# Optimization experiments

Measured on AMD Instinct MI355X. Metric: run time of the kernel, lower is better.

## Reference

```python
import jax, jax.numpy as jnp
import numpy as np


def setup_inputs() -> dict:
    key = jax.random.key(0)
    ks = jax.random.split(key, 8)
    B, S, D, H, E = 4, 2048, 1024, 2048, 8
    s = 0.02  # init scale
    return {
        "x": jax.random.normal(ks[0], (B, S, D), dtype=jnp.float32),
        "gate_w": jax.random.normal(ks[1], (E, D), dtype=jnp.float32) * s,
        "w1": jax.random.normal(ks[2], (E, H, D), dtype=jnp.float32) * s,
        "b1": jnp.zeros((E, H), dtype=jnp.float32),
        "w2": jax.random.normal(ks[3], (E, H, D), dtype=jnp.float32) * s,
        "b2": jnp.zeros((E, H), dtype=jnp.float32),
        "w3": jax.random.normal(ks[4], (E, D, H), dtype=jnp.float32) * s,
        "b3": jnp.zeros((E, D), dtype=jnp.float32),
        "topk": 2,
    }


def reference(x, gate_w, w1, b1, w2, b2, w3, b3, topk):
    D = x.shape[-1]
    E = gate_w.shape[0]
    xf = x.reshape(-1, D)                      # [T, D]
    T = xf.shape[0]

    logits = xf @ gate_w.T                     # [T, E]
    vals, idx = jax.lax.top_k(logits, topk)    # [T, K]
    wts = jax.nn.softmax(vals, axis=-1)        # [T, K]

    # per-token combine weight per expert (0 if expert not in top-k)
    comb = jnp.zeros((T, E), dtype=xf.dtype).at[
        jnp.arange(T)[:, None], idx
    ].add(wts)                                 # [T, E]

    out = jnp.zeros_like(xf)
    for e in range(E):  # fixed small loop over experts
        h = (xf @ w1[e].T + b1[e]) * jax.nn.silu(xf @ w2[e].T + b2[e])  # [T, H]
        y = h @ w3[e].T + b3[e]                                           # [T, D]
        out = out + comb[:, e:e + 1] * y
    return out.reshape(x.shape)
```

## Files before the change

kernel.cpp:

```cpp
#include <hip/hip_runtime.h>
#include <hip/hip_bf16.h>
#include <stdint.h>

#define T_TOK   8192
#define D_DIM   1024
#define H_DIM   2048
#define E_EXP   8
#define NP2     4096
#define BM      256
#define CAP     (2*T_TOK + E_EXP*BM)
#define MAXMB   (CAP/BM)

using f32x4 = __attribute__((ext_vector_type(4))) float;
using s16x4 = __attribute__((ext_vector_type(4))) short;
using s16x8 = __attribute__((ext_vector_type(8))) short;

__device__ __forceinline__ short bf16_of(float f) {
  union { float f; unsigned u; } v; v.f = f;
  unsigned r = v.u + 0x7FFFu + ((v.u >> 16) & 1u);
  return (short)(r >> 16);
}
__device__ __forceinline__ float f_of_bf16(short s) {
  union { unsigned u; float f; } v; v.u = ((unsigned)(unsigned short)s) << 16;
  return v.f;
}

__device__ __forceinline__ void gload16(const void* g, void* l) {
  __builtin_amdgcn_global_load_lds(
      (const __attribute__((address_space(1))) unsigned int*)g,
      (__attribute__((address_space(3))) unsigned int*)l, 16, 0, 0);
}

__global__ __launch_bounds__(256) void conv_w12(const float* __restrict__ w1,
                                                const float* __restrict__ w2,
                                                short* __restrict__ w12b) {
  int idx = blockIdx.x * 256 + threadIdx.x;
  int e = idx >> 20;
  int rem = idx & 0xFFFFF;
  int np = rem >> 8;
  int kc = rem & 255;
  int g = np >> 5, tt = np & 31, half = tt >> 4, srow = g * 16 + (tt & 15);
  const f32x4* src = (const f32x4*)(half ? w2 : w1) + ((size_t)e * H_DIM + srow) * 256 + kc;
  f32x4 v = *src;
  s16x4 o;
  o[0] = bf16_of(v[0]); o[1] = bf16_of(v[1]); o[2] = bf16_of(v[2]); o[3] = bf16_of(v[3]);
  ((s16x4*)w12b)[idx] = o;
}

__global__ __launch_bounds__(256) void conv_w3(const float* __restrict__ w3,
                                               short* __restrict__ w3b) {
  int idx = blockIdx.x * 256 + threadIdx.x;
  f32x4 v = ((const f32x4*)w3)[idx];
  s16x4 o;
  o[0] = bf16_of(v[0]); o[1] = bf16_of(v[1]); o[2] = bf16_of(v[2]); o[3] = bf16_of(v[3]);
  ((s16x4*)w3b)[idx] = o;
}

__global__ __launch_bounds__(256) void gate_kernel(const float* __restrict__ x,
                                                   const float* __restrict__ gw,
                                                   int* __restrict__ tok_e,
                                                   float* __restrict__ gatew) {
  __shared__ float g[E_EXP * D_DIM];
  int tid = threadIdx.x;
  for (int i = tid; i < E_EXP * 256; i += 256)
    ((f32x4*)g)[i] = ((const f32x4*)gw)[i];
  __syncthreads();
  int w = tid >> 6, lane = tid & 63;
  int t = blockIdx.x * 4 + w;
  float acc[E_EXP] = {};
  const f32x4* xrow = (const f32x4*)(x + (size_t)t * D_DIM);
#pragma unroll
  for (int i = 0; i < 4; ++i) {
    f32x4 xv = xrow[lane + 64 * i];
#pragma unroll
    for (int e = 0; e < E_EXP; ++e) {
      f32x4 gv = ((const f32x4*)g)[e * 256 + lane + 64 * i];
      acc[e] += xv[0] * gv[0] + xv[1] * gv[1] + xv[2] * gv[2] + xv[3] * gv[3];
    }
  }
#pragma unroll
  for (int e = 0; e < E_EXP; ++e)
#pragma unroll
    for (int off = 1; off < 64; off <<= 1)
      acc[e] += __shfl_xor(acc[e], off);
  if (lane == 0) {
    int i0 = 0; float v0 = acc[0];
    for (int e = 1; e < E_EXP; ++e) if (acc[e] > v0) { v0 = acc[e]; i0 = e; }
    int i1 = -1; float v1 = -1e30f;
    for (int e = 0; e < E_EXP; ++e) if (e != i0 && acc[e] > v1) { v1 = acc[e]; i1 = e; }
    float z = __expf(v1 - v0);
    tok_e[2 * t] = i0; tok_e[2 * t + 1] = i1;
    gatew[2 * t] = 1.f / (1.f + z); gatew[2 * t + 1] = z / (1.f + z);
  }
}

__global__ __launch_bounds__(256) void hist_kernel(const int* __restrict__ tok_e,
                                                   int* __restrict__ counts) {
  __shared__ int bc[E_EXP];
  const int tid = threadIdx.x, lane = tid & 63;
  if (tid < E_EXP) bc[tid] = 0;
  __syncthreads();
  const int4 v = ((const int4*)tok_e)[blockIdx.x * 256 + tid];
#pragma unroll
  for (int e = 0; e < E_EXP; ++e) {
    int cnt = __popcll(__ballot(v.x == e)) + __popcll(__ballot(v.y == e)) +
              __popcll(__ballot(v.z == e)) + __popcll(__ballot(v.w == e));
    if (lane == 0 && cnt) atomicAdd(&bc[e], cnt);
  }
  __syncthreads();
  if (tid < E_EXP && bc[tid]) atomicAdd(&counts[tid], bc[tid]);
}

__global__ void scan_kernel(const int* __restrict__ counts, int* __restrict__ off,
                            int* __restrict__ mb2e, int* __restrict__ mb2row) {
  if (threadIdx.x == 0 && blockIdx.x == 0) {
    int acc = 0, mb = 0;
    for (int e = 0; e < E_EXP; ++e) {
      off[e] = acc;
      int nb = (counts[e] + BM - 1) / BM;
      for (int b = 0; b < nb; ++b) { mb2e[mb] = e; mb2row[mb] = acc + b * BM; ++mb; }
      acc += nb * BM;
    }
    off[E_EXP] = acc;
    for (; mb < MAXMB; ++mb) mb2e[mb] = -1;
  }
}

__global__ __launch_bounds__(256) void assign_kernel(const int* __restrict__ tok_e,
                                                     const int* __restrict__ off,
                                                     int* __restrict__ fill,
                                                     int* __restrict__ perm,
                                                     int* __restrict__ tok_slot) {
  __shared__ int wcnt[4][E_EXP];
  __shared__ int wbase[4][E_EXP];
  const int tid = threadIdx.x, lane = tid & 63, wid = tid >> 6;
  if (tid < 32) wcnt[tid >> 3][tid & 7] = 0;
  __syncthreads();
  const int ent = blockIdx.x * 256 + tid;
  const int e = tok_e[ent];
  int myrank = 0;
#pragma unroll
  for (int e0 = 0; e0 < E_EXP; ++e0) {
    unsigned long long m = __ballot(e == e0);
    if (e == e0) {
      myrank = __popcll(m & ((1ull << lane) - 1ull));
      if (myrank == 0) wcnt[wid][e0] = __popcll(m);
    }
  }
  __syncthreads();
  if (tid < E_EXP) {
    int tot = wcnt[0][tid] + wcnt[1][tid] + wcnt[2][tid] + wcnt[3][tid];
    int base = tot ? atomicAdd(&fill[tid], tot) : 0;
#pragma unroll
    for (int w = 0; w < 4; ++w) { wbase[w][tid] = base; base += wcnt[w][tid]; }
  }
  __syncthreads();
  const int slot = off[e] + wbase[wid][e] + myrank;
  perm[slot] = ent >> 1;
  tok_slot[ent] = slot;
}

__global__ __launch_bounds__(128) void gather_kernel(const float* __restrict__ x,
                                                     const int* __restrict__ off,
                                                     const int* __restrict__ counts,
                                                     const int* __restrict__ perm,
                                                     short* __restrict__ Xp) {
  int s = blockIdx.x, tid = threadIdx.x;
  int e = -1;
#pragma unroll
  for (int i = 0; i < E_EXP; ++i)
    if (s >= off[i] && s < off[i + 1]) { e = i; break; }
  bool valid = false; int t = 0;
  if (e >= 0) { int r = s - off[e]; if (r < counts[e]) { valid = true; t = perm[s]; } }
  s16x8 o;
  if (valid) {
    const f32x4* xr = (const f32x4*)(x + (size_t)t * D_DIM);
    f32x4 a = xr[tid * 2], b = xr[tid * 2 + 1];
    o[0] = bf16_of(a[0]); o[1] = bf16_of(a[1]); o[2] = bf16_of(a[2]); o[3] = bf16_of(a[3]);
    o[4] = bf16_of(b[0]); o[5] = bf16_of(b[1]); o[6] = bf16_of(b[2]); o[7] = bf16_of(b[3]);
  } else {
#pragma unroll
    for (int j = 0; j < 8; ++j) o[j] = 0;
  }
  *(s16x8*)(Xp + (size_t)s * D_DIM + tid * 8) = o;
}

template <int K, int BN_, int EPI>
__global__ __launch_bounds__(512, (BN_ == 128) ? 4 : 2)
void gemm256(const short* __restrict__ A,
             const short* __restrict__ Bw,
             const int* __restrict__ mb2e,
             const int* __restrict__ mb2row,
             const float* __restrict__ biasA,
             const float* __restrict__ biasB,
             short* __restrict__ Out) {
  constexpr int NFULL = (EPI == 0) ? NP2 : D_DIM;
  constexpr int OUTLD = (EPI == 0) ? H_DIM : D_DIM;
  constexpr int KB = K * 2;
  constexpr int NT = K / 32;
  constexpr int NBF = BN_ / 64;
  constexpr int ABYTES = 16384;
  constexpr int BBYTES = BN_ * 64;
  constexpr int BUFB = ABYTES + BBYTES;
  constexpr int NB_LOADS = BN_ / 128;
  constexpr int INFLIGHT = 2 + NB_LOADS;

  const int mb = blockIdx.y;
  const int e = mb2e[mb];
  if (e < 0) return;
  const int row0 = mb2row[mb];
  const int bn = blockIdx.x;

  __shared__ alignas(16) char lds[3 * BUFB];

  const int tid = threadIdx.x;
  const int lane = tid & 63;
  const int wid = tid >> 6;
  const int wr = wid >> 2;
  const int wc = wid & 3;

  const char* gA = (const char*)(A + (size_t)row0 * K);
  const char* gB = (const char*)(Bw + ((size_t)e * NFULL + (size_t)bn * BN_) * K);

  const int srow0 = tid >> 2, spq = tid & 3;

  f32x4 acc[8][NBF] = {};

  auto stageA = [&](int kt, int buf) {
#pragma unroll
    for (int r = 0; r < 2; ++r) {
      const int row = r * 128 + srow0;
      const int lq = spq ^ ((row >> 1) & 3);
      gload16(gA + (size_t)row * KB + kt * 64 + lq * 16,
              lds + buf * BUFB + r * 8192 + tid * 16);
    }
  };
  auto stageB = [&](int kt, int buf) {
#pragma unroll
    for (int r = 0; r < NB_LOADS; ++r) {
      const int row = r * 128 + srow0;
      const int lq = spq ^ ((row >> 1) & 3);
      gload16(gB + (size_t)row * KB + kt * 64 + lq * 16,
              lds + buf * BUFB + ABYTES + r * 8192 + tid * 16);
    }
  };

  stageA(0, 0); stageB(0, 0);
  stageA(1, 1); stageB(1, 1);
  if constexpr (BN_ == 256) asm volatile("s_waitcnt vmcnt(4)" ::: "memory");
  else                      asm volatile("s_waitcnt vmcnt(3)" ::: "memory");
  __builtin_amdgcn_s_barrier();
  __builtin_amdgcn_sched_barrier(0);

  const int qsw = (((lane >> 4) ^ ((lane >> 1) & 3)) << 4);
  const int arow = wr * 128 + (lane & 15);
  const int brow = wc * (BN_ / 4) + (lane & 15);

  int bc = 0;
  int b2 = 2;
  for (int t = 0; t < NT; ++t) {
    const char* bufb = lds + bc * BUFB;
    const char* pa = bufb + arow * 64 + qsw;
    const char* pb = bufb + ABYTES + brow * 64 + qsw;
    s16x8 av[4], bv[NBF];
#pragma unroll
    for (int f = 0; f < NBF; ++f) bv[f] = *(const s16x8*)(pb + f * 1024);
#pragma unroll
    for (int f = 0; f < 4; ++f) av[f] = *(const s16x8*)(pa + f * 1024);
    if (t + 2 < NT) stageA(t + 2, b2);
    __builtin_amdgcn_s_setprio(1);
#pragma unroll
    for (int mf = 0; mf < 4; ++mf)
#pragma unroll
      for (int nf = 0; nf < NBF; ++nf)
        acc[mf][nf] = __builtin_amdgcn_mfma_f32_16x16x32_bf16(av[mf], bv[nf], acc[mf][nf], 0, 0, 0);
    __builtin_amdgcn_s_setprio(0);
#pragma unroll
    for (int f = 0; f < 4; ++f) av[f] = *(const s16x8*)(pa + (4 + f) * 1024);
    if (t + 2 < NT) stageB(t + 2, b2);
    __builtin_amdgcn_s_setprio(1);
#pragma unroll
    for (int mf = 0; mf < 4; ++mf)
#pragma unroll
      for (int nf = 0; nf < NBF; ++nf)
        acc[4 + mf][nf] = __builtin_amdgcn_mfma_f32_16x16x32_bf16(av[mf], bv[nf], acc[4 + mf][nf], 0, 0, 0);
    __builtin_amdgcn_s_setprio(0);

    if (t < NT - 1) {
      __builtin_amdgcn_sched_barrier(0);
      if (t == NT - 2)          asm volatile("s_waitcnt vmcnt(0)" ::: "memory");
      else if (BN_ == 256)      asm volatile("s_waitcnt vmcnt(4)" ::: "memory");
      else                      asm volatile("s_waitcnt vmcnt(3)" ::: "memory");
      __builtin_amdgcn_s_barrier();
      __builtin_amdgcn_sched_barrier(0);
    }
    bc = (bc == 2) ? 0 : bc + 1;
    b2 = (b2 == 2) ? 0 : b2 + 1;
  }

  if constexpr (EPI == 0) {
#pragma unroll
    for (int mf = 0; mf < 8; ++mf) {
      const int mrow = row0 + wr * 128 + mf * 16 + ((lane >> 4) << 2);
#pragma unroll
      for (int p = 0; p < 2; ++p) {
        const int hcol = bn * 128 + wc * 32 + p * 16 + (lane & 15);
        const float bb1 = biasA[e * H_DIM + hcol];
        const float bb2 = biasB[e * H_DIM + hcol];
        const f32x4 a1 = acc[mf][2 * p], a2 = acc[mf][2 * p + 1];
#pragma unroll
        for (int j = 0; j < 4; ++j) {
          float x1 = a1[j] + bb1, x2 = a2[j] + bb2;
          float hv = x1 * (x2 / (1.f + __expf(-x2)));
          Out[(size_t)(mrow + j) * OUTLD + hcol] = bf16_of(hv);
        }
      }
    }
  } else {
#pragma unroll
    for (int mf = 0; mf < 8; ++mf) {
      const int mrow = row0 + wr * 128 + mf * 16 + ((lane >> 4) << 2);
#pragma unroll
      for (int nf = 0; nf < NBF; ++nf) {
        const int col = bn * BN_ + wc * (BN_ / 4) + nf * 16 + (lane & 15);
        const float bb = biasA[e * D_DIM + col];
#pragma unroll
        for (int j = 0; j < 4; ++j)
          Out[(size_t)(mrow + j) * OUTLD + col] = bf16_of(acc[mf][nf][j] + bb);
      }
    }
  }
}

__global__ __launch_bounds__(128) void combine_kernel(const short* __restrict__ ysb,
                                                      const int* __restrict__ tok_slot,
                                                      const float* __restrict__ gatew,
                                                      float* __restrict__ out) {
  int t = blockIdx.x, tid = threadIdx.x;
  int s0 = tok_slot[2 * t], s1 = tok_slot[2 * t + 1];
  float w0 = gatew[2 * t], w1 = gatew[2 * t + 1];
  s16x8 a = *(const s16x8*)(ysb + (size_t)s0 * D_DIM + tid * 8);
  s16x8 b = *(const s16x8*)(ysb + (size_t)s1 * D_DIM + tid * 8);
  float* op = out + (size_t)t * D_DIM + tid * 8;
  f32x4 o0, o1;
#pragma unroll
  for (int j = 0; j < 4; ++j) o0[j] = w0 * f_of_bf16(a[j]) + w1 * f_of_bf16(b[j]);
#pragma unroll
  for (int j = 0; j < 4; ++j) o1[j] = w0 * f_of_bf16(a[4 + j]) + w1 * f_of_bf16(b[4 + j]);
  *(f32x4*)op = o0;
  *(f32x4*)(op + 4) = o1;
}

extern "C" void kernel_launch(void* const* d_in, const int* in_sizes, int n_in,
                              void* d_out, int out_size, void* d_ws, size_t ws_size,
                              hipStream_t stream) {
  const float* x  = (const float*)d_in[0];
  const float* gw = (const float*)d_in[1];
  const float* w1 = (const float*)d_in[2];
  const float* b1 = (const float*)d_in[3];
  const float* w2 = (const float*)d_in[4];
  const float* b2 = (const float*)d_in[5];
  const float* w3 = (const float*)d_in[6];
  const float* b3 = (const float*)d_in[7];
  float* out = (float*)d_out;

  char* ws = (char*)d_ws;
  size_t o = 0;
  short* w12b = (short*)(ws + o); o += (size_t)E_EXP * NP2 * D_DIM * 2;
  short* w3b  = (short*)(ws + o); o += (size_t)E_EXP * D_DIM * H_DIM * 2;
  short* Xp   = (short*)(ws + o); o += (size_t)CAP * D_DIM * 2;
  short* ysb  = Xp;
  short* hbuf = (short*)(ws + o); o += (size_t)CAP * H_DIM * 2;
  int* meta     = (int*)(ws + o);
  int* counts   = meta;
  int* fill     = meta + 8;
  int* offv     = meta + 16;
  int* mb2e     = meta + 32;
  int* mb2row   = meta + 112;
  int* tok_e    = meta + 192;
  int* tok_slot = tok_e + 2 * T_TOK;
  int* perm     = tok_slot + 2 * T_TOK;
  float* gatew  = (float*)(perm + CAP);
  const size_t ws_needed = o + (192 + 4 * T_TOK + CAP + 2 * T_TOK) * sizeof(int);
  if (ws_size < ws_needed) return;

  hipMemsetAsync(counts, 0, 16 * sizeof(int), stream);

  conv_w12<<<(E_EXP * NP2 * 256) / 256, 256, 0, stream>>>(w1, w2, w12b);
  conv_w3 <<<(E_EXP * D_DIM * (H_DIM / 4)) / 256, 256, 0, stream>>>(w3, w3b);
  gate_kernel<<<T_TOK / 4, 256, 0, stream>>>(x, gw, tok_e, gatew);
  hist_kernel<<<(2 * T_TOK) / 1024, 256, 0, stream>>>(tok_e, counts);
  scan_kernel<<<1, 64, 0, stream>>>(counts, offv, mb2e, mb2row);
  assign_kernel<<<(2 * T_TOK) / 256, 256, 0, stream>>>(tok_e, offv, fill, perm, tok_slot);
  gather_kernel<<<CAP, 128, 0, stream>>>(x, offv, counts, perm, Xp);
  gemm256<D_DIM, 256, 0><<<dim3(NP2 / 256, MAXMB), 512, 0, stream>>>(Xp, w12b, mb2e, mb2row, b1, b2, hbuf);
  gemm256<H_DIM, 128, 1><<<dim3(D_DIM / 128, MAXMB), 512, 0, stream>>>(hbuf, w3b, mb2e, mb2row, b3, b3, ysb);
  combine_kernel<<<T_TOK, 128, 0, stream>>>(ysb, tok_slot, gatew, out);
}
```

Baseline: 383.5 us.

## Fuse weighted combine into down-projection GEMM epilogue via atomic adds

Removes the separate combine kernel. The second GEMM's epilogue now scales each row by its gate weight and atomically adds it straight into the zero-initialised fp32 output, using the permutation and per-slot weights written by the assign kernel. The down-projection tile width also grows from 128 to 256 columns, with lower occupancy in exchange for more reuse. This drops the bf16 intermediate round trip and one kernel launch, but adds a full output memset, uncoalesced per-element fp32 atomics, and a grid cut to 4 column blocks per row block.

```diff
diff --git a/kernel.cpp b/kernel.cpp
--- a/kernel.cpp
+++ b/kernel.cpp
@@ -127,10 +127,11 @@
 }
 
 __global__ __launch_bounds__(256) void assign_kernel(const int* __restrict__ tok_e,
+                                                     const float* __restrict__ gatew,
                                                      const int* __restrict__ off,
                                                      int* __restrict__ fill,
                                                      int* __restrict__ perm,
-                                                     int* __restrict__ tok_slot) {
+                                                     float* __restrict__ wslot) {
   __shared__ int wcnt[4][E_EXP];
   __shared__ int wbase[4][E_EXP];
   const int tid = threadIdx.x, lane = tid & 63, wid = tid >> 6;
@@ -157,7 +158,7 @@
   __syncthreads();
   const int slot = off[e] + wbase[wid][e] + myrank;
   perm[slot] = ent >> 1;
-  tok_slot[ent] = slot;
+  wslot[slot] = gatew[ent];
 }
 
 __global__ __launch_bounds__(128) void gather_kernel(const float* __restrict__ x,
@@ -185,25 +186,25 @@
   *(s16x8*)(Xp + (size_t)s * D_DIM + tid * 8) = o;
 }
 
-template <int K, int BN_, int EPI>
-__global__ __launch_bounds__(512, (BN_ == 128) ? 4 : 2)
+template <int K, int EPI>
+__global__ __launch_bounds__(512, 2)
 void gemm256(const short* __restrict__ A,
              const short* __restrict__ Bw,
              const int* __restrict__ mb2e,
              const int* __restrict__ mb2row,
              const float* __restrict__ biasA,
              const float* __restrict__ biasB,
-             short* __restrict__ Out) {
+             short* __restrict__ Out,
+             const int* __restrict__ permv,
+             const float* __restrict__ wslot,
+             const int* __restrict__ offv,
+             const int* __restrict__ cnts,
+             float* __restrict__ outp) {
   constexpr int NFULL = (EPI == 0) ? NP2 : D_DIM;
-  constexpr int OUTLD = (EPI == 0) ? H_DIM : D_DIM;
   constexpr int KB = K * 2;
   constexpr int NT = K / 32;
-  constexpr int NBF = BN_ / 64;
   constexpr int ABYTES = 16384;
-  constexpr int BBYTES = BN_ * 64;
-  constexpr int BUFB = ABYTES + BBYTES;
-  constexpr int NB_LOADS = BN_ / 128;
-  constexpr int INFLIGHT = 2 + NB_LOADS;
+  constexpr int BUFB = 2 * ABYTES;
 
   const int mb = blockIdx.y;
   const int e = mb2e[mb];
@@ -220,11 +221,11 @@
   const int wc = wid & 3;
 
   const char* gA = (const char*)(A + (size_t)row0 * K);
-  const char* gB = (const char*)(Bw + ((size_t)e * NFULL + (size_t)bn * BN_) * K);
+  const char* gB = (const char*)(Bw + ((size_t)e * NFULL + (size_t)bn * 256) * K);
 
   const int srow0 = tid >> 2, spq = tid & 3;
 
-  f32x4 acc[8][NBF] = {};
+  f32x4 acc[8][4] = {};
 
   auto stageA = [&](int kt, int buf) {
 #pragma unroll
@@ -237,7 +238,7 @@
   };
   auto stageB = [&](int kt, int buf) {
 #pragma unroll
-    for (int r = 0; r < NB_LOADS; ++r) {
+    for (int r = 0; r < 2; ++r) {
       const int row = r * 128 + srow0;
       const int lq = spq ^ ((row >> 1) & 3);
       gload16(gB + (size_t)row * KB + kt * 64 + lq * 16,
@@ -247,14 +248,13 @@
 
   stageA(0, 0); stageB(0, 0);
   stageA(1, 1); stageB(1, 1);
-  if constexpr (BN_ == 256) asm volatile("s_waitcnt vmcnt(4)" ::: "memory");
-  else                      asm volatile("s_waitcnt vmcnt(3)" ::: "memory");
+  asm volatile("s_waitcnt vmcnt(4)" ::: "memory");
   __builtin_amdgcn_s_barrier();
   __builtin_amdgcn_sched_barrier(0);
 
   const int qsw = (((lane >> 4) ^ ((lane >> 1) & 3)) << 4);
   const int arow = wr * 128 + (lane & 15);
-  const int brow = wc * (BN_ / 4) + (lane & 15);
+  const int brow = wc * 64 + (lane & 15);
 
   int bc = 0;
   int b2 = 2;
@@ -262,9 +262,9 @@
     const char* bufb = lds + bc * BUFB;
     const char* pa = bufb + arow * 64 + qsw;
     const char* pb = bufb + ABYTES + brow * 64 + qsw;
-    s16x8 av[4], bv[NBF];
-#pragma unroll
-    for (int f = 0; f < NBF; ++f) bv[f] = *(const s16x8*)(pb + f * 1024);
+    s16x8 av[4], bv[4];
+#pragma unroll
+    for (int f = 0; f < 4; ++f) bv[f] = *(const s16x8*)(pb + f * 1024);
 #pragma unroll
     for (int f = 0; f < 4; ++f) av[f] = *(const s16x8*)(pa + f * 1024);
     if (t + 2 < NT) stageA(t + 2, b2);
@@ -272,7 +272,7 @@
 #pragma unroll
     for (int mf = 0; mf < 4; ++mf)
 #pragma unroll
-      for (int nf = 0; nf < NBF; ++nf)
+      for (int nf = 0; nf < 4; ++nf)
         acc[mf][nf] = __builtin_amdgcn_mfma_f32_16x16x32_bf16(av[mf], bv[nf], acc[mf][nf], 0, 0, 0);
     __builtin_amdgcn_s_setprio(0);
 #pragma unroll
@@ -282,15 +282,14 @@
 #pragma unroll
     for (int mf = 0; mf < 4; ++mf)
 #pragma unroll
-      for (int nf = 0; nf < NBF; ++nf)
+      for (int nf = 0; nf < 4; ++nf)
         acc[4 + mf][nf] = __builtin_amdgcn_mfma_f32_16x16x32_bf16(av[mf], bv[nf], acc[4 + mf][nf], 0, 0, 0);
     __builtin_amdgcn_s_setprio(0);
 
     if (t < NT - 1) {
       __builtin_amdgcn_sched_barrier(0);
-      if (t == NT - 2)          asm volatile("s_waitcnt vmcnt(0)" ::: "memory");
-      else if (BN_ == 256)      asm volatile("s_waitcnt vmcnt(4)" ::: "memory");
-      else                      asm volatile("s_waitcnt vmcnt(3)" ::: "memory");
+      if (t == NT - 2) asm volatile("s_waitcnt vmcnt(0)" ::: "memory");
+      else             asm volatile("s_waitcnt vmcnt(4)" ::: "memory");
       __builtin_amdgcn_s_barrier();
       __builtin_amdgcn_sched_barrier(0);
     }
@@ -312,43 +311,35 @@
         for (int j = 0; j < 4; ++j) {
           float x1 = a1[j] + bb1, x2 = a2[j] + bb2;
           float hv = x1 * (x2 / (1.f + __expf(-x2)));
-          Out[(size_t)(mrow + j) * OUTLD + hcol] = bf16_of(hv);
+          Out[(size_t)(mrow + j) * H_DIM + hcol] = bf16_of(hv);
         }
       }
     }
   } else {
+    const int ebase = offv[e];
+    const int ecnt = cnts[e];
 #pragma unroll
     for (int mf = 0; mf < 8; ++mf) {
       const int mrow = row0 + wr * 128 + mf * 16 + ((lane >> 4) << 2);
-#pragma unroll
-      for (int nf = 0; nf < NBF; ++nf) {
-        const int col = bn * BN_ + wc * (BN_ / 4) + nf * 16 + (lane & 15);
+      int tok[4]; float wg[4]; bool val[4];
+#pragma unroll
+      for (int j = 0; j < 4; ++j) {
+        const int s = mrow + j;
+        val[j] = (s - ebase) < ecnt;
+        tok[j] = val[j] ? permv[s] : 0;
+        wg[j]  = val[j] ? wslot[s] : 0.f;
+      }
+#pragma unroll
+      for (int nf = 0; nf < 4; ++nf) {
+        const int col = bn * 256 + wc * 64 + nf * 16 + (lane & 15);
         const float bb = biasA[e * D_DIM + col];
 #pragma unroll
         for (int j = 0; j < 4; ++j)
-          Out[(size_t)(mrow + j) * OUTLD + col] = bf16_of(acc[mf][nf][j] + bb);
+          if (val[j])
+            atomicAdd(&outp[(size_t)tok[j] * D_DIM + col], wg[j] * (acc[mf][nf][j] + bb));
       }
     }
   }
-}
-
-__global__ __launch_bounds__(128) void combine_kernel(const short* __restrict__ ysb,
-                                                      const int* __restrict__ tok_slot,
-                                                      const float* __restrict__ gatew,
-                                                      float* __restrict__ out) {
-  int t = blockIdx.x, tid = threadIdx.x;
-  int s0 = tok_slot[2 * t], s1 = tok_slot[2 * t + 1];
-  float w0 = gatew[2 * t], w1 = gatew[2 * t + 1];
-  s16x8 a = *(const s16x8*)(ysb + (size_t)s0 * D_DIM + tid * 8);
-  s16x8 b = *(const s16x8*)(ysb + (size_t)s1 * D_DIM + tid * 8);
-  float* op = out + (size_t)t * D_DIM + tid * 8;
-  f32x4 o0, o1;
-#pragma unroll
-  for (int j = 0; j < 4; ++j) o0[j] = w0 * f_of_bf16(a[j]) + w1 * f_of_bf16(b[j]);
-#pragma unroll
-  for (int j = 0; j < 4; ++j) o1[j] = w0 * f_of_bf16(a[4 + j]) + w1 * f_of_bf16(b[4 + j]);
-  *(f32x4*)op = o0;
-  *(f32x4*)(op + 4) = o1;
 }
 
 extern "C" void kernel_launch(void* const* d_in, const int* in_sizes, int n_in,
@@ -369,7 +360,6 @@
   short* w12b = (short*)(ws + o); o += (size_t)E_EXP * NP2 * D_DIM * 2;
   short* w3b  = (short*)(ws + o); o += (size_t)E_EXP * D_DIM * H_DIM * 2;
   short* Xp   = (short*)(ws + o); o += (size_t)CAP * D_DIM * 2;
-  short* ysb  = Xp;
   short* hbuf = (short*)(ws + o); o += (size_t)CAP * H_DIM * 2;
   int* meta     = (int*)(ws + o);
   int* counts   = meta;
@@ -378,22 +368,24 @@
   int* mb2e     = meta + 32;
   int* mb2row   = meta + 112;
   int* tok_e    = meta + 192;
-  int* tok_slot = tok_e + 2 * T_TOK;
-  int* perm     = tok_slot + 2 * T_TOK;
+  int* perm     = tok_e + 2 * T_TOK;
   float* gatew  = (float*)(perm + CAP);
-  const size_t ws_needed = o + (192 + 4 * T_TOK + CAP + 2 * T_TOK) * sizeof(int);
+  float* wslot  = gatew + 2 * T_TOK;
+  const size_t ws_needed = o + (192 + 2 * T_TOK + CAP + 2 * T_TOK + CAP) * sizeof(int);
   if (ws_size < ws_needed) return;
 
   hipMemsetAsync(counts, 0, 16 * sizeof(int), stream);
+  hipMemsetAsync(out, 0, (size_t)T_TOK * D_DIM * sizeof(float), stream);
 
   conv_w12<<<(E_EXP * NP2 * 256) / 256, 256, 0, stream>>>(w1, w2, w12b);
   conv_w3 <<<(E_EXP * D_DIM * (H_DIM / 4)) / 256, 256, 0, stream>>>(w3, w3b);
   gate_kernel<<<T_TOK / 4, 256, 0, stream>>>(x, gw, tok_e, gatew);
   hist_kernel<<<(2 * T_TOK) / 1024, 256, 0, stream>>>(tok_e, counts);
   scan_kernel<<<1, 64, 0, stream>>>(counts, offv, mb2e, mb2row);
-  assign_kernel<<<(2 * T_TOK) / 256, 256, 0, stream>>>(tok_e, offv, fill, perm, tok_slot);
+  assign_kernel<<<(2 * T_TOK) / 256, 256, 0, stream>>>(tok_e, gatew, offv, fill, perm, wslot);
   gather_kernel<<<CAP, 128, 0, stream>>>(x, offv, counts, perm, Xp);
-  gemm256<D_DIM, 256, 0><<<dim3(NP2 / 256, MAXMB), 512, 0, stream>>>(Xp, w12b, mb2e, mb2row, b1, b2, hbuf);
-  gemm256<H_DIM, 128, 1><<<dim3(D_DIM / 128, MAXMB), 512, 0, stream>>>(hbuf, w3b, mb2e, mb2row, b3, b3, ysb);
-  combine_kernel<<<T_TOK, 128, 0, stream>>>(ysb, tok_slot, gatew, out);
-}
+  gemm256<D_DIM, 0><<<dim3(NP2 / 256, MAXMB), 512, 0, stream>>>(
+      Xp, w12b, mb2e, mb2row, b1, b2, hbuf, nullptr, nullptr, nullptr, nullptr, nullptr);
+  gemm256<H_DIM, 2><<<dim3(D_DIM / 256, MAXMB), 512, 0, stream>>>(
+      hbuf, w3b, mb2e, mb2row, b3, b3, nullptr, perm, wslot, offv, counts, out);
+}
```

Result: slower. 473.9 us (+23.6%).
